# Kernel optimization log

Measured on AMD Instinct MI355X. Metric: run time of the kernel, lower is better.

## Reference

```python
import jax, jax.numpy as jnp
import numpy as np

N_NODES = 50000


def setup_inputs() -> dict:
    key = jax.random.key(0)
    k1, k2, k3, k4 = jax.random.split(key, 4)
    in_c, out_c = 128, 128
    x = jax.random.normal(k1, (N_NODES, in_c), dtype=jnp.float32)
    edge_index = jax.random.randint(k2, (2, 600000), 0, N_NODES, dtype=jnp.int64)
    W_l = jax.random.normal(k3, (out_c, in_c), dtype=jnp.float32) / np.sqrt(in_c)
    W_r = jax.random.normal(k4, (out_c, in_c), dtype=jnp.float32) / np.sqrt(in_c)
    b = jnp.zeros((out_c,), dtype=jnp.float32)
    return {"x": x, "edge_index": edge_index, "W_l": W_l, "W_r": W_r, "b": b}


def reference(x, edge_index, W_l, W_r, b):
    # SAGEConv (PyG defaults): mean aggregation over incoming neighbors,
    # out = lin_l(mean_agg) + lin_r(x) + bias, then log_softmax over features.
    src, dst = edge_index[0], edge_index[1]
    msgs = x[src]  # [E, in_c] gather of source features
    summed = jax.ops.segment_sum(msgs, dst, num_segments=N_NODES)  # [N, in_c]
    counts = jax.ops.segment_sum(jnp.ones_like(dst, dtype=x.dtype), dst,
                                 num_segments=N_NODES)  # [N]
    agg = summed / jnp.maximum(counts, 1.0)[:, None]  # mean; 0 for isolated nodes
    out = agg @ W_l.T + x @ W_r.T + b  # [N, out_c]
    return jax.nn.log_softmax(out, axis=1)
```

## Files before the change

### kernel.cpp

```cpp
#include <hip/hip_runtime.h>
#include <cmath>

#define C   128
#define PAD 64

typedef __bf16 bf16x8 __attribute__((ext_vector_type(8)));
typedef float  f32x4  __attribute__((ext_vector_type(4)));
typedef unsigned short u16x8 __attribute__((ext_vector_type(8)));

static __device__ __forceinline__ unsigned short f2b(float f) {
    unsigned int u = __builtin_bit_cast(unsigned int, f);
    u += 0x7FFFu + ((u >> 16) & 1u);
    return (unsigned short)(u >> 16);
}
static __device__ __forceinline__ float b2f(unsigned short u) {
    return __builtin_bit_cast(float, (unsigned int)u << 16);
}

__global__ __launch_bounds__(256)
void sage_init(const float* __restrict__ Wl, const float* __restrict__ Wr,
               int4* __restrict__ counts4, unsigned short* __restrict__ wp,
               int n4, int ZB) {
    int bid = blockIdx.x;
    int t = threadIdx.x;
    if (bid < ZB) {
        int i = bid * 256 + t;
        if (i < n4) counts4[i] = make_int4(0, 0, 0, 0);
    } else {
        int s = (bid - ZB) * 256 + t;
        int f = s >> 6, l = s & 63;
        int kt = f >> 4, mt = f & 15;
        int g = l >> 4;
        int m = mt * 16 + (l & 15);
        const float* src = (m < C) ? (Wl + (size_t)m * C)
                                   : (Wr + (size_t)(m - C) * C);
        u16x8 o;
#pragma unroll
        for (int j = 0; j < 8; ++j) o[j] = f2b(src[kt * 32 + g * 8 + j]);
        *(u16x8*)(wp + (size_t)s * 8) = o;
    }
}

__global__ __launch_bounds__(256)
void sage_fill_gemm(const float* __restrict__ x,
                    const unsigned short* __restrict__ wp,
                    const float* __restrict__ bias,
                    const int* __restrict__ ei,
                    int* __restrict__ counts, unsigned short* __restrict__ csr,
                    unsigned short* __restrict__ yl,
                    unsigned short* __restrict__ yr,
                    int N, int E, int FB) {
    int bid = blockIdx.x;
    int t = threadIdx.x;

    if (bid < FB) {
        int e = bid * 256 + t;
        if (e < E) {
            int src = ei[e];
            int dst = ei[E + e];
            int k = atomicAdd(&counts[dst], 1);
            if (k < PAD) csr[(size_t)dst * PAD + k] = (unsigned short)src;
        }
        return;
    }

    int w = t >> 6, l = t & 63;
    int g = l >> 4;

    int node = (bid - FB) * 16 + (l & 15);
    if (node >= N) node = N - 1;
    const float4* xv = (const float4*)(x + (size_t)node * C);
    const bf16x8* A = (const bf16x8*)wp;

    f32x4 acc0 = {0.f,0.f,0.f,0.f}, acc1 = {0.f,0.f,0.f,0.f};
    f32x4 acc2 = {0.f,0.f,0.f,0.f}, acc3 = {0.f,0.f,0.f,0.f};

#pragma unroll
    for (int kt = 0; kt < 4; ++kt) {
        float4 xa = xv[kt * 8 + g * 2];
        float4 xc = xv[kt * 8 + g * 2 + 1];
        u16x8 ab;
        ab[0]=f2b(xa.x); ab[1]=f2b(xa.y); ab[2]=f2b(xa.z); ab[3]=f2b(xa.w);
        ab[4]=f2b(xc.x); ab[5]=f2b(xc.y); ab[6]=f2b(xc.z); ab[7]=f2b(xc.w);
        bf16x8 xf = __builtin_bit_cast(bf16x8, ab);
        int c = w * 4;
        bf16x8 a0 = A[(size_t)(kt * 16 + c + 0) * 64 + l];
        bf16x8 a1 = A[(size_t)(kt * 16 + c + 1) * 64 + l];
        bf16x8 a2 = A[(size_t)(kt * 16 + c + 2) * 64 + l];
        bf16x8 a3 = A[(size_t)(kt * 16 + c + 3) * 64 + l];
        acc0 = __builtin_amdgcn_mfma_f32_16x16x32_bf16(a0, xf, acc0, 0,0,0);
        acc1 = __builtin_amdgcn_mfma_f32_16x16x32_bf16(a1, xf, acc1, 0,0,0);
        acc2 = __builtin_amdgcn_mfma_f32_16x16x32_bf16(a2, xf, acc2, 0,0,0);
        acc3 = __builtin_amdgcn_mfma_f32_16x16x32_bf16(a3, xf, acc3, 0,0,0);
    }

    size_t rowoff = (size_t)node * C;
#pragma unroll
    for (int i = 0; i < 4; ++i) {
        f32x4 a = (i == 0) ? acc0 : (i == 1) ? acc1 : (i == 2) ? acc2 : acc3;
        int mt = w * 4 + i;
        float4 bv = (mt >= 8) ? *(const float4*)(bias + (mt - 8) * 16 + g * 4)
                              : make_float4(0.f, 0.f, 0.f, 0.f);
        ushort4 o;
        o.x = f2b(a[0] + bv.x);
        o.y = f2b(a[1] + bv.y);
        o.z = f2b(a[2] + bv.z);
        o.w = f2b(a[3] + bv.w);
        unsigned short* yp = (mt < 8) ? yl : yr;
        *(ushort4*)(yp + rowoff + (mt & 7) * 16 + g * 4) = o;
    }
}

__global__ __launch_bounds__(256)
void sage_final(const unsigned short* __restrict__ yl,
                const unsigned short* __restrict__ yr,
                const int* __restrict__ counts,
                const unsigned short* __restrict__ csr,
                float* __restrict__ out, int N) {
    int wv = threadIdx.x >> 6;
    int node = blockIdx.x * 4 + wv;
    if (node >= N) return;
    int ln = threadIdx.x & 63;
    int q = ln >> 4;
    int fl = ln & 15;

    int deg = counts[node];
    deg = (deg > PAD) ? PAD : deg;
    int p0 = node * PAD;
    int p1 = p0 + deg;

    float a[8];
#pragma unroll
    for (int j = 0; j < 8; ++j) a[j] = 0.f;

    int p = p0 + q;
    for (; p + 12 < p1; p += 16) {
        int s0 = csr[p], s1 = csr[p + 4], s2 = csr[p + 8], s3 = csr[p + 12];
        u16x8 v0 = *(const u16x8*)(yl + (size_t)s0 * C + fl * 8);
        u16x8 v1 = *(const u16x8*)(yl + (size_t)s1 * C + fl * 8);
        u16x8 v2 = *(const u16x8*)(yl + (size_t)s2 * C + fl * 8);
        u16x8 v3 = *(const u16x8*)(yl + (size_t)s3 * C + fl * 8);
#pragma unroll
        for (int j = 0; j < 8; ++j)
            a[j] += (b2f(v0[j]) + b2f(v1[j])) + (b2f(v2[j]) + b2f(v3[j]));
    }
    for (; p + 4 < p1; p += 8) {
        int s0 = csr[p], s1 = csr[p + 4];
        u16x8 v0 = *(const u16x8*)(yl + (size_t)s0 * C + fl * 8);
        u16x8 v1 = *(const u16x8*)(yl + (size_t)s1 * C + fl * 8);
#pragma unroll
        for (int j = 0; j < 8; ++j) a[j] += b2f(v0[j]) + b2f(v1[j]);
    }
    if (p < p1) {
        int s0 = csr[p];
        u16x8 v0 = *(const u16x8*)(yl + (size_t)s0 * C + fl * 8);
#pragma unroll
        for (int j = 0; j < 8; ++j) a[j] += b2f(v0[j]);
    }

#pragma unroll
    for (int j = 0; j < 8; ++j) {
        a[j] += __shfl_xor(a[j], 16);
        a[j] += __shfl_xor(a[j], 32);
    }
    if (q != 0) return;

    float inv = 1.0f / fmaxf((float)deg, 1.0f);
    u16x8 yv = *(const u16x8*)(yr + (size_t)node * C + fl * 8);
#pragma unroll
    for (int j = 0; j < 8; ++j) a[j] = a[j] * inv + b2f(yv[j]);

    float m = a[0];
#pragma unroll
    for (int j = 1; j < 8; ++j) m = fmaxf(m, a[j]);
#pragma unroll
    for (int off = 1; off < 16; off <<= 1)
        m = fmaxf(m, __shfl_xor(m, off));
    float s = 0.f;
#pragma unroll
    for (int j = 0; j < 8; ++j) s += expf(a[j] - m);
#pragma unroll
    for (int off = 1; off < 16; off <<= 1)
        s += __shfl_xor(s, off);
    float ls = m + logf(s);

    float4 o0, o1;
    o0.x = a[0] - ls; o0.y = a[1] - ls; o0.z = a[2] - ls; o0.w = a[3] - ls;
    o1.x = a[4] - ls; o1.y = a[5] - ls; o1.z = a[6] - ls; o1.w = a[7] - ls;
    float4* op = (float4*)(out + (size_t)node * C + fl * 8);
    op[0] = o0;
    op[1] = o1;
}

extern "C" void kernel_launch(void* const* d_in, const int* in_sizes, int n_in,
                              void* d_out, int out_size, void* d_ws, size_t ws_size,
                              hipStream_t stream) {
    const float* x  = (const float*)d_in[0];
    const int*   ei = (const int*)d_in[1];
    const float* Wl = (const float*)d_in[2];
    const float* Wr = (const float*)d_in[3];
    const float* b  = (const float*)d_in[4];
    float* out = (float*)d_out;

    const int N = in_sizes[0] / C;
    const int E = in_sizes[1] / 2;

    int* counts = (int*)d_ws;
    unsigned short* csr = (unsigned short*)(counts + ((N + 3) & ~3));
    unsigned short* yl  = csr + (size_t)N * PAD;
    unsigned short* yr  = yl + (size_t)N * C;
    unsigned short* wp  = yr + (size_t)N * C;

    int n4 = (N + 3) / 4;
    const int ZB = (n4 + 255) / 256;
    const int FB = (E + 255) / 256;
    const int NT = (N + 15) / 16;

    sage_init<<<ZB + 16, 256, 0, stream>>>(Wl, Wr, (int4*)counts, wp, n4, ZB);
    sage_fill_gemm<<<FB + NT, 256, 0, stream>>>(x, wp, b, ei, counts, csr,
                                                yl, yr, N, E, FB);
    sage_final<<<(N + 3) / 4, 256, 0, stream>>>(yl, yr, counts, csr, out, N);
}
```

Before: 101.5 us.

## Partition CSR fill by destination range per XCD to localize atomics

The edge-fill blocks are now replicated once per XCD (8 copies), and each copy processes only edges whose destination falls in that XCD's node range. Since blocks are assigned to XCDs round-robin, all atomics and CSR writes for a node come from one XCD and stay in that die's L2. Each thread also reads 8 edges with vectorized int4 loads. The cost is reading the whole edge list eight times and launching more blocks.

New measurement: 97.84 us. -3.6%, faster.

```diff
diff --git a/kernel.cpp b/kernel.cpp
--- a/kernel.cpp
+++ b/kernel.cpp
@@ -1,8 +1,9 @@
 #include <hip/hip_runtime.h>
 #include <cmath>
 
-#define C   128
-#define PAD 64
+#define C    128
+#define PAD  64
+#define NXCD 8
 
 typedef __bf16 bf16x8 __attribute__((ext_vector_type(8)));
 typedef float  f32x4  __attribute__((ext_vector_type(4)));
@@ -54,12 +55,36 @@
     int t = threadIdx.x;
 
     if (bid < FB) {
-        int e = bid * 256 + t;
-        if (e < E) {
-            int src = ei[e];
-            int dst = ei[E + e];
-            int k = atomicAdd(&counts[dst], 1);
-            if (k < PAD) csr[(size_t)dst * PAD + k] = (unsigned short)src;
+        int xcd = bid & (NXCD - 1);
+        int chunk = bid >> 3;
+        int span = (N + NXCD - 1) / NXCD;
+        int lo = xcd * span;
+        int hi = min(N, lo + span);
+        int e0 = (chunk * 256 + t) * 8;
+        if (e0 + 7 < E) {
+            int4 d0 = *(const int4*)(ei + E + e0);
+            int4 d1 = *(const int4*)(ei + E + e0 + 4);
+            int4 s0 = *(const int4*)(ei + e0);
+            int4 s1 = *(const int4*)(ei + e0 + 4);
+            int dd[8] = {d0.x, d0.y, d0.z, d0.w, d1.x, d1.y, d1.z, d1.w};
+            int ss[8] = {s0.x, s0.y, s0.z, s0.w, s1.x, s1.y, s1.z, s1.w};
+#pragma unroll
+            for (int j = 0; j < 8; ++j) {
+                if (dd[j] >= lo && dd[j] < hi) {
+                    int k = atomicAdd(&counts[dd[j]], 1);
+                    if (k < PAD)
+                        csr[(size_t)dd[j] * PAD + k] = (unsigned short)ss[j];
+                }
+            }
+        } else {
+            for (int e = e0; e < E; ++e) {
+                int dst = ei[E + e];
+                if (dst >= lo && dst < hi) {
+                    int k = atomicAdd(&counts[dst], 1);
+                    if (k < PAD)
+                        csr[(size_t)dst * PAD + k] = (unsigned short)ei[e];
+                }
+            }
         }
         return;
     }
@@ -213,7 +238,8 @@
 
     int n4 = (N + 3) / 4;
     const int ZB = (n4 + 255) / 256;
-    const int FB = (E + 255) / 256;
+    const int NCH = (E + 2047) / 2048;
+    const int FB = NCH * NXCD;
     const int NT = (N + 15) / 16;
 
     sage_init<<<ZB + 16, 256, 0, stream>>>(Wl, Wr, (int4*)counts, wp, n4, ZB);
```

## Partition CSR fill by destination range per XCD and interleave with GEMM tiles

Applied to the files above, without the earlier changes.

The edge-scatter phase is restructured so each group of 16 blocks has 8 fill blocks, each owning one eighth of the destination-node range, interleaved with 8 GEMM tile blocks. The intent is that with round-robin block-to-XCD placement, atomics and CSR writes for a given node range stay on one XCD's L2, which cuts cross-die coherence traffic. The cost is that every fill block reads all its edges and discards 7/8 of them, so edge-index reads rise eightfold. Edges are now read in int2 pairs.

Result: slower. 108.0 us (+6.5%).

```diff
diff --git a/kernel.cpp b/kernel.cpp
--- a/kernel.cpp
+++ b/kernel.cpp
@@ -1,8 +1,9 @@
 #include <hip/hip_runtime.h>
 #include <cmath>
 
-#define C   128
-#define PAD 64
+#define C    128
+#define PAD  64
+#define NXCD 8
 
 typedef __bf16 bf16x8 __attribute__((ext_vector_type(8)));
 typedef float  f32x4  __attribute__((ext_vector_type(4)));
@@ -49,25 +50,48 @@
                     int* __restrict__ counts, unsigned short* __restrict__ csr,
                     unsigned short* __restrict__ yl,
                     unsigned short* __restrict__ yr,
-                    int N, int E, int FB) {
+                    int N, int E, int NCH, int NT) {
     int bid = blockIdx.x;
     int t = threadIdx.x;
-
-    if (bid < FB) {
-        int e = bid * 256 + t;
-        if (e < E) {
-            int src = ei[e];
-            int dst = ei[E + e];
-            int k = atomicAdd(&counts[dst], 1);
-            if (k < PAD) csr[(size_t)dst * PAD + k] = (unsigned short)src;
+    int group = bid >> 4;
+    int pos = bid & 15;
+
+    if (pos < 8) {
+        if (group >= NCH) return;
+        int span = (N + NXCD - 1) / NXCD;
+        int lo = pos * span;
+        int hi = min(N, lo + span);
+        int e0 = (group * 256 + t) * 2;
+        if (e0 + 1 < E) {
+            int2 dv = *(const int2*)(ei + E + e0);
+            int2 sv = *(const int2*)(ei + e0);
+            if (dv.x >= lo && dv.x < hi) {
+                int k = atomicAdd(&counts[dv.x], 1);
+                if (k < PAD) csr[(size_t)dv.x * PAD + k] = (unsigned short)sv.x;
+            }
+            if (dv.y >= lo && dv.y < hi) {
+                int k = atomicAdd(&counts[dv.y], 1);
+                if (k < PAD) csr[(size_t)dv.y * PAD + k] = (unsigned short)sv.y;
+            }
+        } else if (e0 < E) {
+            for (int e = e0; e < E; ++e) {
+                int dst = ei[E + e];
+                if (dst >= lo && dst < hi) {
+                    int k = atomicAdd(&counts[dst], 1);
+                    if (k < PAD) csr[(size_t)dst * PAD + k] = (unsigned short)ei[e];
+                }
+            }
         }
         return;
     }
 
+    int tile = group * 8 + (pos - 8);
+    if (tile >= NT) return;
+
     int w = t >> 6, l = t & 63;
     int g = l >> 4;
 
-    int node = (bid - FB) * 16 + (l & 15);
+    int node = tile * 16 + (l & 15);
     if (node >= N) node = N - 1;
     const float4* xv = (const float4*)(x + (size_t)node * C);
     const bf16x8* A = (const bf16x8*)wp;
@@ -213,11 +237,12 @@
 
     int n4 = (N + 3) / 4;
     const int ZB = (n4 + 255) / 256;
-    const int FB = (E + 255) / 256;
+    const int NCH = (E + 511) / 512;
     const int NT = (N + 15) / 16;
+    const int NGRP = (NCH > (NT + 7) / 8) ? NCH : (NT + 7) / 8;
 
     sage_init<<<ZB + 16, 256, 0, stream>>>(Wl, Wr, (int4*)counts, wp, n4, ZB);
-    sage_fill_gemm<<<FB + NT, 256, 0, stream>>>(x, wp, b, ei, counts, csr,
-                                                yl, yr, N, E, FB);
+    sage_fill_gemm<<<NGRP * 16, 256, 0, stream>>>(x, wp, b, ei, counts, csr,
+                                                  yl, yr, N, E, NCH, NT);
     sage_final<<<(N + 3) / 4, 256, 0, stream>>>(yl, yr, counts, csr, out, N);
 }
```
